# Kernel optimization log

Measured on AMD Instinct MI355X. Metric: run time of the kernel, lower is better.

Reference implementation:

```python
import jax, jax.numpy as jnp
import numpy as np
from jax import lax

C = 128; H = 28; W = 28
VID_LENS = [32, 96, 64, 48, 80, 40, 88, 64]  # sums to 512
T_TOTAL = sum(VID_LENS)


def setup_inputs() -> dict:
    key = jax.random.key(0)
    ks = jax.random.split(key, 6)
    fan2 = C * 9
    fan1 = C * 3
    return {
        "x": jax.random.normal(ks[0], (T_TOTAL, C, H, W), dtype=jnp.float32),
        "vid_lens": jnp.array(VID_LENS, dtype=jnp.int32),
        "w_sp": jax.random.normal(ks[1], (C, C, 3, 3), dtype=jnp.float32) / np.sqrt(fan2),
        "b_sp": jax.random.normal(ks[2], (C,), dtype=jnp.float32) * 0.01,
        "w_t": jax.random.normal(ks[3], (C, C, 3), dtype=jnp.float32) / np.sqrt(fan1),
        "b_t": jax.random.normal(ks[4], (C,), dtype=jnp.float32) * 0.01,
        "alpha": jnp.full((C,), 0.25, dtype=jnp.float32),  # MultiNL ~ per-channel PReLU
    }


def _forward(x, vid_lens, w_sp, b_sp, w_t, b_t, alpha):
    projection = x
    # spatial 3x3 conv, stride 1, padding 1 (SAME), NCHW
    y = lax.conv_general_dilated(
        x, w_sp, window_strides=(1, 1), padding="SAME",
        dimension_numbers=("NCHW", "OIHW", "NCHW")) + b_sp[None, :, None, None]

    # Ragged temporal conv1d (k=3, pad=1) over concatenated time axis.
    # Zero the temporal neighbors at segment boundaries so each video is
    # convolved independently (equivalent to per-segment zero padding).
    T = y.shape[0]
    ends = jnp.cumsum(vid_lens)            # segment end indices (exclusive)
    starts = ends - vid_lens               # segment start indices
    start_mask = jnp.zeros((T,), bool).at[starts].set(True)
    end_mask = jnp.zeros((T,), bool).at[ends - 1].set(True)

    y_prev = jnp.where(start_mask[:, None, None, None], 0.0, jnp.roll(y, 1, axis=0))
    y_next = jnp.where(end_mask[:, None, None, None], 0.0, jnp.roll(y, -1, axis=0))

    # conv1d along time == per-tap channel-mixing matmul
    z = (jnp.einsum("oc,tchw->tohw", w_t[:, :, 0], y_prev)
         + jnp.einsum("oc,tchw->tohw", w_t[:, :, 1], y)
         + jnp.einsum("oc,tchw->tohw", w_t[:, :, 2], y_next)
         + b_t[None, :, None, None])

    # MultiNL modeled as per-channel PReLU
    z = jnp.where(z >= 0, z, alpha[None, :, None, None] * z)
    return z + projection


def reference(x, vid_lens, w_sp, b_sp, w_t, b_t, alpha):
    out = _forward(x, vid_lens, w_sp, b_sp, w_t, b_t, alpha)
    return (out, vid_lens)  # lengths are unchanged (k=3, pad=1)
```

## Files before the change

kernel.cpp:

```cpp
#include <hip/hip_runtime.h>

#define TT   512
#define CH   128
#define HWP  784
#define NSEG 8
#define NOUT 51380224

typedef short bf16x8  __attribute__((ext_vector_type(8)));
typedef float f32x4   __attribute__((ext_vector_type(4)));
typedef int   i32x4   __attribute__((ext_vector_type(4)));
typedef unsigned short u16x8 __attribute__((ext_vector_type(8)));

__device__ inline unsigned short f2bf(float f) {
    unsigned u = __builtin_bit_cast(unsigned, f);
    u += 0x7fffu + ((u >> 16) & 1u);
    return (unsigned short)(u >> 16);
}

__device__ inline void gld_lds16(const void* g, void* l) {
    __builtin_amdgcn_global_load_lds(
        (const __attribute__((address_space(1))) void*)g,
        (__attribute__((address_space(3))) void*)l, 16, 0, 0);
}

__global__ void repack_wsp(const float* __restrict__ w, short* __restrict__ wA) {
    int s = blockIdx.x * 256 + threadIdx.x;
    if (s >= 128 * 128 * 9) return;
    int co = s / 1152, r = s % 1152, ci = r / 9, kh = (r % 9) / 3, kw = r % 3;
    int tap = kh * 3 + kw;
    int dst = tap * 16384 + (co >> 4) * 2048 + (ci >> 5) * 512 +
              ((ci >> 3) & 3) * 128 + (co & 15) * 8 + (ci & 7);
    wA[dst] = (short)f2bf(w[s]);
}

__global__ void repack_wt2(const float* __restrict__ w, short* __restrict__ wAt) {
    int s = blockIdx.x * 256 + threadIdx.x;
    if (s >= 128 * 128 * 3) return;
    int o = s / 384, r = s % 384, k = r / 3, tap = r % 3;
    int ci = (k & 96) | (((k >> 2) & 1) << 4) | (((k >> 3) & 3) << 2) | (k & 3);
    int dst = tap * 16384 + (o >> 4) * 2048 + (k >> 5) * 512 +
              ((k >> 3) & 3) * 128 + (o & 15) * 8 + (k & 7);
    wAt[dst] = (short)f2bf(w[o * 384 + ci * 3 + tap]);
}

__global__ __launch_bounds__(512, 4) void spatial_mfma(
    const float* __restrict__ x, const short* __restrict__ wA,
    const float* __restrict__ b_sp, unsigned short* __restrict__ yT)
{
    __shared__ __align__(16) short xs[300 * 128];
    char* xsb = (char*)xs;
    const int t = blockIdx.y, blockh = blockIdx.x * 8;
    const int tid = threadIdx.x;

    for (int it = 0; it < 3; ++it) {
        int u = it * 512 + tid;
        if (u < 1280) {
            int cp = u & 63, rs = u >> 6;
            int st = (rs >> 1) * 30 + (rs & 1) * 29;
            int addr = (st << 8) | (cp << 2);
            addr ^= ((st ^ (st >> 4)) & 15) << 4;
            *(unsigned*)(xsb + addr) = 0u;
        }
    }
    for (int it = 0; it < 9; ++it) {
        int u = it * 512 + tid;
        if (u < 4480) {
            int cp = u & 63, pq = u >> 6;
            int rl = pq / 7, g = pq % 7;
            int rr = blockh - 1 + rl;
            float4 f0 = make_float4(0.f, 0.f, 0.f, 0.f), f1 = f0;
            if (rr >= 0 && rr < 28) {
                const float* p0 = &x[((size_t)(t * CH + 2 * cp)) * HWP + rr * 28 + g * 4];
                f0 = *(const float4*)p0;
                f1 = *(const float4*)(p0 + HWP);
            }
            float a0[4] = {f0.x, f0.y, f0.z, f0.w}, a1[4] = {f1.x, f1.y, f1.z, f1.w};
            int stb = rl * 30 + g * 4 + 1;
#pragma unroll
            for (int j = 0; j < 4; ++j) {
                int st = stb + j;
                unsigned val = (unsigned)f2bf(a0[j]) | ((unsigned)f2bf(a1[j]) << 16);
                int addr = (st << 8) | (cp << 2);
                addr ^= ((st ^ (st >> 4)) & 15) << 4;
                *(unsigned*)(xsb + addr) = val;
            }
        }
    }
    __syncthreads();

    const int wid = tid >> 6, l = tid & 63;
    const int wm = wid & 1, rg = (wid >> 1) & 1, ms = wid >> 2;
    const int l15 = l & 15, kgrp = l >> 4;
    const int h0 = blockh + rg * 4;
    if (h0 >= 28) return;

    int st0[7];
#pragma unroll
    for (int nf = 0; nf < 7; ++nf) {
        int pl = nf * 16 + l15;
        st0[nf] = (rg * 4 + pl / 28 + 1) * 30 + (pl % 28) + 1;
    }

    f32x4 acc[2][7];
#pragma unroll
    for (int d = 0; d < 2; ++d)
#pragma unroll
        for (int n = 0; n < 7; ++n) acc[d][n] = (f32x4){0.f, 0.f, 0.f, 0.f};

    const bf16x8* wAv = (const bf16x8*)wA;

    for (int tap = 0; tap < 9; ++tap) {
        int off = (tap / 3 - 1) * 30 + (tap % 3 - 1);
        int adr[7];
#pragma unroll
        for (int nf = 0; nf < 7; ++nf) {
            int st = st0[nf] + off;
            adr[nf] = ((st << 8) | (kgrp << 4)) ^ (((st ^ (st >> 4)) & 15) << 4);
        }
#pragma unroll
        for (int ks = 0; ks < 4; ++ks) {
            bf16x8 a0 = wAv[((tap * 8 + wm * 4 + ms * 2 + 0) * 4 + ks) * 64 + l];
            bf16x8 a1 = wAv[((tap * 8 + wm * 4 + ms * 2 + 1) * 4 + ks) * 64 + l];
            __builtin_amdgcn_s_setprio(1);
#pragma unroll
            for (int nf = 0; nf < 7; ++nf) {
                i32x4 bi = *(const i32x4*)(xsb + (adr[nf] ^ (ks << 6)));
                bf16x8 b = __builtin_bit_cast(bf16x8, bi);
                acc[0][nf] = __builtin_amdgcn_mfma_f32_16x16x32_bf16(a0, b, acc[0][nf], 0, 0, 0);
                acc[1][nf] = __builtin_amdgcn_mfma_f32_16x16x32_bf16(a1, b, acc[1][nf], 0, 0, 0);
            }
            __builtin_amdgcn_s_setprio(0);
        }
    }

    float4 blo = *(const float4*)&b_sp[wm * 64 + ms * 32 + kgrp * 4];
    float4 bhi = *(const float4*)&b_sp[wm * 64 + ms * 32 + 16 + kgrp * 4];
    float bl[4] = {blo.x, blo.y, blo.z, blo.w}, bh[4] = {bhi.x, bhi.y, bhi.z, bhi.w};
#pragma unroll
    for (int nf = 0; nf < 7; ++nf) {
        int px = h0 * 28 + nf * 16 + l15;
        u16x8 pk;
#pragma unroll
        for (int r = 0; r < 4; ++r) {
            pk[r]     = f2bf(acc[0][nf][r] + bl[r]);
            pk[4 + r] = f2bf(acc[1][nf][r] + bh[r]);
        }
        char* dst = (char*)yT + ((size_t)t * HWP + px) * 256 + wm * 128 + ms * 64 + kgrp * 16;
        *(u16x8*)dst = pk;
    }
}

__global__ __launch_bounds__(256, 4) void temporal_mfma(
    const unsigned short* __restrict__ yT, const short* __restrict__ wAt,
    const float* __restrict__ b_t, const float* __restrict__ alpha,
    const float* __restrict__ x, const int* __restrict__ vid_lens,
    float* __restrict__ out)
{
    __shared__ __align__(16) char ldsT[29696];

    const int chunk = blockIdx.x, t = blockIdx.y;
    const int tid = threadIdx.x, wid = tid >> 6, l = tid & 63;
    const int l15 = l & 15, kgrp = l >> 4;
    const int sx = l15 & 7;

    bool isS = false, isE = false;
    {
        int cum = 0;
        for (int s = 0; s < NSEG; ++s) {
            if (t == cum) isS = true;
            cum += vid_lens[s];
            if (t == cum - 1) isE = true;
        }
    }
    const bool tapAct[3] = {!isS, true, !isE};

    auto stage = [&](int s) {
        int tap = s >> 1, kp = s & 1;
        if (!tapAct[tap]) return;
        int tp = t + tap - 1;
        const char* yb = (const char*)yT + (size_t)tp * HWP * 256;
        char* buf = ldsT + (s & 1) * 14336;
#pragma unroll
        for (int r = 0; r < 4; ++r) {
            int c = r * 256 + wid * 64 + l;
            if (r < 3 || wid < 2) {
                int px = c >> 3, sp = c & 7;
                int ssrc = sp ^ (px & 7);
                const char* g = yb + ((size_t)(chunk * 112 + px)) * 256 + kp * 128 + ssrc * 16;
                char* ldst = buf + (r * 256 + wid * 64) * 16;
                gld_lds16(g, ldst);
            }
        }
    };

    f32x4 acc[2][7];
#pragma unroll
    for (int m = 0; m < 2; ++m)
#pragma unroll
        for (int n = 0; n < 7; ++n) acc[m][n] = (f32x4){0.f, 0.f, 0.f, 0.f};

    const bf16x8* wAv = (const bf16x8*)wAt;

    stage(0);
    __syncthreads();

    for (int s = 0; s < 6; ++s) {
        if (s < 5) stage(s + 1);
        int tap = s >> 1, kp = s & 1;
        if (tapAct[tap]) {
            const char* buf = ldsT + (s & 1) * 14336;
            bf16x8 a[2][2];
#pragma unroll
            for (int m = 0; m < 2; ++m)
#pragma unroll
                for (int k1 = 0; k1 < 2; ++k1)
                    a[m][k1] = wAv[((tap * 8 + wid * 2 + m) * 4 + kp * 2 + k1) * 64 + l];
            __builtin_amdgcn_s_setprio(1);
#pragma unroll
            for (int k1 = 0; k1 < 2; ++k1) {
#pragma unroll
                for (int nf = 0; nf < 7; ++nf) {
                    int addr = (nf * 16 + l15) * 128 + ((k1 * 4 + kgrp) ^ sx) * 16;
                    i32x4 bi = *(const i32x4*)(buf + addr);
                    bf16x8 b = __builtin_bit_cast(bf16x8, bi);
                    acc[0][nf] = __builtin_amdgcn_mfma_f32_16x16x32_bf16(a[0][k1], b, acc[0][nf], 0, 0, 0);
                    acc[1][nf] = __builtin_amdgcn_mfma_f32_16x16x32_bf16(a[1][k1], b, acc[1][nf], 0, 0, 0);
                }
            }
            __builtin_amdgcn_s_setprio(0);
        }
        __syncthreads();
    }

    float* fl = (float*)ldsT;
    const int wbase = wid * 1856;
#pragma unroll
    for (int m = 0; m < 2; ++m) {
#pragma unroll
        for (int nf = 0; nf < 7; ++nf)
#pragma unroll
            for (int rr = 0; rr < 4; ++rr)
                fl[wbase + (kgrp * 4 + rr) * 116 + nf * 16 + l15] = acc[m][nf][rr];
#pragma unroll
        for (int j = 0; j < 7; ++j) {
            int idx = j * 64 + l;
            int co_r = idx / 28, q = idx % 28;
            f32x4 v4 = *(const f32x4*)&fl[wbase + co_r * 116 + q * 4];
            int co_g = wid * 32 + m * 16 + co_r;
            float bt = b_t[co_g], al = alpha[co_g];
            size_t gi = ((size_t)(t * CH + co_g)) * HWP + chunk * 112 + q * 4;
            float4 xv = *(const float4*)&x[gi];
            float xr[4] = {xv.x, xv.y, xv.z, xv.w};
            float rrv[4];
#pragma unroll
            for (int e = 0; e < 4; ++e) {
                float v = v4[e] + bt;
                v = (v >= 0.f) ? v : al * v;
                rrv[e] = v + xr[e];
            }
            *(float4*)&out[gi] = make_float4(rrv[0], rrv[1], rrv[2], rrv[3]);
        }
        __syncthreads();
    }
}

__global__ void write_lens(const int* __restrict__ vid_lens, float* __restrict__ out) {
    int i = threadIdx.x;
    if (i < NSEG) out[NOUT + i] = (float)vid_lens[i];
}

extern "C" void kernel_launch(void* const* d_in, const int* in_sizes, int n_in,
                              void* d_out, int out_size, void* d_ws, size_t ws_size,
                              hipStream_t stream) {
    const float* x        = (const float*)d_in[0];
    const int*   vid_lens = (const int*)d_in[1];
    const float* w_sp     = (const float*)d_in[2];
    const float* b_sp     = (const float*)d_in[3];
    const float* w_t      = (const float*)d_in[4];
    const float* b_t      = (const float*)d_in[5];
    const float* alpha    = (const float*)d_in[6];
    float* out = (float*)d_out;

    unsigned short* yT = (unsigned short*)d_ws;
    short* wA  = (short*)((char*)d_ws + 102760448);
    short* wAt = (short*)((char*)d_ws + 102760448 + 294912);

    repack_wsp<<<576, 256, 0, stream>>>(w_sp, wA);
    repack_wt2<<<192, 256, 0, stream>>>(w_t, wAt);
    spatial_mfma<<<dim3(4, 512), 512, 0, stream>>>(x, wA, b_sp, yT);
    temporal_mfma<<<dim3(7, 512), 256, 0, stream>>>(yT, wAt, b_t, alpha, x, vid_lens, out);
    write_lens<<<1, 64, 0, stream>>>(vid_lens, out);
}
```

Measured before the change: 297.7 us.

## Switch spatial conv to 32x32x16 MFMA tiles with per-wave pixel partitioning

Rewrites the spatial conv inner loop so each wave owns 32 pixels and all 128 output channels, accumulating with 32x32x16 bf16 MFMAs instead of 16x16x32. The weight repack layout and LDS swizzle change to match, and the temporal weight repack is simplified. The aim is fewer LDS B-fragment loads per MFMA and better MFMA throughput. The cost is that each wave now loads all four weight fragments per k-step, and the last wave of the bottom row block sits idle or partially masked.

```diff
diff --git a/kernel.cpp b/kernel.cpp
--- a/kernel.cpp
+++ b/kernel.cpp
@@ -8,8 +8,9 @@
 
 typedef short bf16x8  __attribute__((ext_vector_type(8)));
 typedef float f32x4   __attribute__((ext_vector_type(4)));
+typedef float f32x16  __attribute__((ext_vector_type(16)));
 typedef int   i32x4   __attribute__((ext_vector_type(4)));
-typedef unsigned short u16x8 __attribute__((ext_vector_type(8)));
+typedef unsigned short u16x4 __attribute__((ext_vector_type(4)));
 
 __device__ inline unsigned short f2bf(float f) {
     unsigned u = __builtin_bit_cast(unsigned, f);
@@ -28,19 +29,20 @@
     if (s >= 128 * 128 * 9) return;
     int co = s / 1152, r = s % 1152, ci = r / 9, kh = (r % 9) / 3, kw = r % 3;
     int tap = kh * 3 + kw;
-    int dst = tap * 16384 + (co >> 4) * 2048 + (ci >> 5) * 512 +
-              ((ci >> 3) & 3) * 128 + (co & 15) * 8 + (ci & 7);
+    int m = co >> 5, row = co & 31;
+    int ks = ci >> 4, kgrp = (ci >> 3) & 1, e = ci & 7;
+    int lane = kgrp * 32 + row;
+    int dst = (((tap * 8 + ks) * 4 + m) * 64 + lane) * 8 + e;
     wA[dst] = (short)f2bf(w[s]);
 }
 
 __global__ void repack_wt2(const float* __restrict__ w, short* __restrict__ wAt) {
     int s = blockIdx.x * 256 + threadIdx.x;
     if (s >= 128 * 128 * 3) return;
-    int o = s / 384, r = s % 384, k = r / 3, tap = r % 3;
-    int ci = (k & 96) | (((k >> 2) & 1) << 4) | (((k >> 3) & 3) << 2) | (k & 3);
-    int dst = tap * 16384 + (o >> 4) * 2048 + (k >> 5) * 512 +
-              ((k >> 3) & 3) * 128 + (o & 15) * 8 + (k & 7);
-    wAt[dst] = (short)f2bf(w[o * 384 + ci * 3 + tap]);
+    int o = s / 384, r = s % 384, i = r / 3, tap = r % 3;
+    int dst = tap * 16384 + (o >> 4) * 2048 + (i >> 5) * 512 +
+              ((i >> 3) & 3) * 128 + (o & 15) * 8 + (i & 7);
+    wAt[dst] = (short)f2bf(w[s]);
 }
 
 __global__ __launch_bounds__(512, 4) void spatial_mfma(
@@ -57,8 +59,7 @@
         if (u < 1280) {
             int cp = u & 63, rs = u >> 6;
             int st = (rs >> 1) * 30 + (rs & 1) * 29;
-            int addr = (st << 8) | (cp << 2);
-            addr ^= ((st ^ (st >> 4)) & 15) << 4;
+            int addr = (st << 8) | ((((cp >> 2) ^ (st & 7)) << 4)) | ((cp & 3) << 2);
             *(unsigned*)(xsb + addr) = 0u;
         }
     }
@@ -80,8 +81,7 @@
             for (int j = 0; j < 4; ++j) {
                 int st = stb + j;
                 unsigned val = (unsigned)f2bf(a0[j]) | ((unsigned)f2bf(a1[j]) << 16);
-                int addr = (st << 8) | (cp << 2);
-                addr ^= ((st ^ (st >> 4)) & 15) << 4;
+                int addr = (st << 8) | ((((cp >> 2) ^ (st & 7)) << 4)) | ((cp & 3) << 2);
                 *(unsigned*)(xsb + addr) = val;
             }
         }
@@ -89,64 +89,59 @@
     __syncthreads();
 
     const int wid = tid >> 6, l = tid & 63;
-    const int wm = wid & 1, rg = (wid >> 1) & 1, ms = wid >> 2;
-    const int l15 = l & 15, kgrp = l >> 4;
-    const int h0 = blockh + rg * 4;
-    if (h0 >= 28) return;
-
-    int st0[7];
-#pragma unroll
-    for (int nf = 0; nf < 7; ++nf) {
-        int pl = nf * 16 + l15;
-        st0[nf] = (rg * 4 + pl / 28 + 1) * 30 + (pl % 28) + 1;
-    }
-
-    f32x4 acc[2][7];
-#pragma unroll
-    for (int d = 0; d < 2; ++d)
-#pragma unroll
-        for (int n = 0; n < 7; ++n) acc[d][n] = (f32x4){0.f, 0.f, 0.f, 0.f};
-
-    const bf16x8* wAv = (const bf16x8*)wA;
+    const int l31 = l & 31, bb5 = l >> 5;
+    int rows = 28 - blockh; if (rows > 8) rows = 8;
+    const int pxcnt = rows * 28;
+    const int p0 = wid * 32;
+    if (wid >= 7 || p0 >= pxcnt) return;
+
+    const int p = p0 + l31;
+    const int st0 = (p / 28 + 1) * 30 + (p % 28) + 1;
+    const bool pok = (p < pxcnt);
+
+    f32x16 zz = {};
+    f32x16 acc0 = zz, acc1 = zz, acc2 = zz, acc3 = zz;
+
+    const bf16x8* wv = (const bf16x8*)wA;
 
     for (int tap = 0; tap < 9; ++tap) {
-        int off = (tap / 3 - 1) * 30 + (tap % 3 - 1);
-        int adr[7];
-#pragma unroll
-        for (int nf = 0; nf < 7; ++nf) {
-            int st = st0[nf] + off;
-            adr[nf] = ((st << 8) | (kgrp << 4)) ^ (((st ^ (st >> 4)) & 15) << 4);
-        }
-#pragma unroll
-        for (int ks = 0; ks < 4; ++ks) {
-            bf16x8 a0 = wAv[((tap * 8 + wm * 4 + ms * 2 + 0) * 4 + ks) * 64 + l];
-            bf16x8 a1 = wAv[((tap * 8 + wm * 4 + ms * 2 + 1) * 4 + ks) * 64 + l];
+        int off = (tap / 3 - 1) * 30 + (tap % 3) - 1;
+        int stv = st0 + off;
+        int rb = stv << 8;
+        int tt = (bb5 ^ (stv & 7)) << 4;
+#pragma unroll
+        for (int ks = 0; ks < 8; ++ks) {
+            int fb = ((tap * 8 + ks) * 4) * 64 + l;
+            bf16x8 a0 = wv[fb];
+            bf16x8 a1 = wv[fb + 64];
+            bf16x8 a2 = wv[fb + 128];
+            bf16x8 a3 = wv[fb + 192];
+            i32x4 bi = *(const i32x4*)(xsb + (rb | ((ks << 5) ^ tt)));
+            bf16x8 bfr = __builtin_bit_cast(bf16x8, bi);
             __builtin_amdgcn_s_setprio(1);
-#pragma unroll
-            for (int nf = 0; nf < 7; ++nf) {
-                i32x4 bi = *(const i32x4*)(xsb + (adr[nf] ^ (ks << 6)));
-                bf16x8 b = __builtin_bit_cast(bf16x8, bi);
-                acc[0][nf] = __builtin_amdgcn_mfma_f32_16x16x32_bf16(a0, b, acc[0][nf], 0, 0, 0);
-                acc[1][nf] = __builtin_amdgcn_mfma_f32_16x16x32_bf16(a1, b, acc[1][nf], 0, 0, 0);
-            }
+            acc0 = __builtin_amdgcn_mfma_f32_32x32x16_bf16(a0, bfr, acc0, 0, 0, 0);
+            acc1 = __builtin_amdgcn_mfma_f32_32x32x16_bf16(a1, bfr, acc1, 0, 0, 0);
+            acc2 = __builtin_amdgcn_mfma_f32_32x32x16_bf16(a2, bfr, acc2, 0, 0, 0);
+            acc3 = __builtin_amdgcn_mfma_f32_32x32x16_bf16(a3, bfr, acc3, 0, 0, 0);
             __builtin_amdgcn_s_setprio(0);
         }
     }
 
-    float4 blo = *(const float4*)&b_sp[wm * 64 + ms * 32 + kgrp * 4];
-    float4 bhi = *(const float4*)&b_sp[wm * 64 + ms * 32 + 16 + kgrp * 4];
-    float bl[4] = {blo.x, blo.y, blo.z, blo.w}, bh[4] = {bhi.x, bhi.y, bhi.z, bhi.w};
-#pragma unroll
-    for (int nf = 0; nf < 7; ++nf) {
-        int px = h0 * 28 + nf * 16 + l15;
-        u16x8 pk;
-#pragma unroll
-        for (int r = 0; r < 4; ++r) {
-            pk[r]     = f2bf(acc[0][nf][r] + bl[r]);
-            pk[4 + r] = f2bf(acc[1][nf][r] + bh[r]);
-        }
-        char* dst = (char*)yT + ((size_t)t * HWP + px) * 256 + wm * 128 + ms * 64 + kgrp * 16;
-        *(u16x8*)dst = pk;
+    const size_t rowbase = ((size_t)t * HWP + blockh * 28 + p) * CH;
+    f32x16 accs[4] = {acc0, acc1, acc2, acc3};
+#pragma unroll
+    for (int m = 0; m < 4; ++m) {
+#pragma unroll
+        for (int r2 = 0; r2 < 4; ++r2) {
+            int cb = m * 32 + 8 * r2 + 4 * bb5;
+            float4 bs = *(const float4*)&b_sp[cb];
+            float bsa[4] = {bs.x, bs.y, bs.z, bs.w};
+            u16x4 pk;
+#pragma unroll
+            for (int q = 0; q < 4; ++q)
+                pk[q] = f2bf(accs[m][r2 * 4 + q] + bsa[q]);
+            if (pok) *(u16x4*)&yT[rowbase + cb] = pk;
+        }
     }
 }
 
```

After: 380.7 us. +27.9%, slower.
